# Kernel tuning notes

Measured on AMD Instinct MI355X. Metric: run time of the kernel, lower is better.

The kernel has to match this reference:

```python
import jax, jax.numpy as jnp
import numpy as np

MAX_IT = 20
LAMBDA_ROF = 7.0
SIGMA = 1.0 / (7.0 * 0.01)
TAU = 0.01
THETA = 0.5

H, W_DIM = 4096, 4096


def forward_weighted_gradient(x, w):
    # x: (1,H,W), w: (2,H,W) -> (2,H,W)
    x0 = x[0]
    gh = jnp.pad(x0[:, 1:] - x0[:, :-1], ((0, 0), (0, 1)))   # grad[0,:, :-1]
    gv = jnp.pad(x0[1:, :] - x0[:-1, :], ((0, 1), (0, 0)))   # grad[1,:-1,:]
    return jnp.stack([gh, gv], axis=0) * w


def backward_divergence(y):
    # y: (2,H,W) -> (1,H,W)
    yh, yv = y[0], y[1]
    d_h = jnp.concatenate(
        [yh[:, :1], yh[:, 1:-1] - yh[:, :-2], -yh[:, -2:-1]], axis=1)
    d_v = jnp.concatenate(
        [yv[:1, :], yv[1:-1, :] - yv[:-2, :], -yv[-2:-1, :]], axis=0)
    return (d_h + d_v)[None]


def prox_linf_ball(p, r):
    # p - detach(max(p-r,0) - max(-p-r,0))  (clamp treated as data in torch code)
    shrink = jnp.maximum(p - r, 0.0) - jnp.maximum(-p - r, 0.0)
    return p - jax.lax.stop_gradient(shrink)


def setup_inputs() -> dict:
    key = jax.random.key(0)
    k1, _ = jax.random.split(key)
    img_obs = jax.random.uniform(k1, (1, H, W_DIM), dtype=jnp.float32)
    w = jnp.ones((2, H, W_DIM), dtype=jnp.float32)
    return {"img_obs": img_obs, "w": w}


def reference(img_obs, w):
    x0 = img_obs
    x_tilde0 = img_obs
    y0 = jnp.zeros((2,) + img_obs.shape[1:], dtype=img_obs.dtype)

    def step(carry, _):
        x, x_tilde, y = carry
        y = y + SIGMA * forward_weighted_gradient(x_tilde, w)
        y = prox_linf_ball(y, 1.0)
        x_old = x
        x = (x + TAU * backward_divergence(y)
             + LAMBDA_ROF * TAU * img_obs) / (1.0 + LAMBDA_ROF * TAU)
        x_tilde = x + THETA * (x - x_old)
        return (x, x_tilde, y), None

    (x, x_tilde, y), _ = jax.lax.scan(step, (x0, x_tilde0, y0), None, length=MAX_IT)
    return x_tilde
```

## Files before the change

### kernel.cpp

```cpp
#include <hip/hip_runtime.h>

static constexpr int H = 4096;
static constexpr int W = 4096;
static constexpr long N = (long)H * W;

static constexpr int TILE = 64;
static constexpr int HOFF = 12;
static constexpr int R    = TILE + 2*HOFF;
static constexpr int CPR  = R / 8;
static constexpr int PR   = R / 2;
static constexpr int NTASK= PR * CPR;
static constexpr int PSE  = PR * R;
static constexpr int NT   = 512;

static constexpr float SIGMA = 14.285714285714286f;
static constexpr float INVD  = 1.0f / 1.07f;
static constexpr float TIV   = 0.01f / 1.07f;
static constexpr float CF    = 0.07f / 1.07f;

typedef _Float16 half8  __attribute__((ext_vector_type(8)));
typedef _Float16 half4v __attribute__((ext_vector_type(4)));

__device__ __forceinline__ half8 splat8(float f) {
    _Float16 h = (_Float16)f;
    half8 v = {h, h, h, h, h, h, h, h};
    return v;
}
__device__ __forceinline__ half8 clamp8(half8 v) {
    v = __builtin_elementwise_min(v, splat8(1.0f));
    v = __builtin_elementwise_max(v, splat8(-1.0f));
    return v;
}
__device__ __forceinline__ half4v lo4(half8 v) {
    half4v r = {v[0], v[1], v[2], v[3]}; return r;
}
__device__ __forceinline__ half4v hi4(half8 v) {
    half4v r = {v[4], v[5], v[6], v[7]}; return r;
}

__global__ __launch_bounds__(256) void pack_w(
    const float* __restrict__ wg,
    _Float16* __restrict__ whp, _Float16* __restrict__ wvp)
{
    const long p = ((long)blockIdx.x * 256 + threadIdx.x) * 8;
    const int i = (int)(p >> 12);
    const float4* hp = reinterpret_cast<const float4*>(wg + p);
    float4 a = hp[0], b = hp[1];
    const float4* vp = reinterpret_cast<const float4*>(wg + N + p);
    float4 c = vp[0], d = vp[1];
    float wh[8] = {a.x, a.y, a.z, a.w, b.x, b.y, b.z, b.w};
    float wv[8] = {c.x, c.y, c.z, c.w, d.x, d.y, d.z, d.w};
    half8 whv, wvv;
#pragma unroll
    for (int k = 0; k < 8; ++k) {
        whv[k] = (_Float16)(SIGMA * wh[k]);
        wvv[k] = (_Float16)(SIGMA * wv[k]);
    }
    if ((p & 4095) + 8 == W) whv[7] = (_Float16)0.0f;
    if (i == H - 1) wvv = splat8(0.0f);
    *reinterpret_cast<half8*>(whp + p) = whv;
    *reinterpret_cast<half8*>(wvp + p) = wvv;
}

template<int PHASE>
__global__ __launch_bounds__(NT, 4) void fused_pd(
    const float* __restrict__ img,
    const _Float16* __restrict__ whp, const _Float16* __restrict__ wvp,
    _Float16* __restrict__ cig,
    _Float16* __restrict__ xg, _Float16* __restrict__ yhg, _Float16* __restrict__ yvg,
    float* __restrict__ out)
{
    __shared__ _Float16 lds_s[2 * PSE + 3 * (NTASK + 2)];
    _Float16* __restrict__ xte  = lds_s;
    _Float16* __restrict__ yvo  = lds_s + PSE;
    _Float16* __restrict__ yheA = lds_s + 2 * PSE;
    _Float16* __restrict__ yheB = yheA + (NTASK + 2);
    _Float16* __restrict__ xteo = yheB + (NTASK + 2);

    const int tid = threadIdx.x;
    const bool act = tid < NTASK;
    const int t  = act ? tid : 0;
    const int p  = t / CPR;
    const int j0 = (t - p * CPR) * 8;
    const int be = p * R + j0;
    const int gi0 = blockIdx.y * TILE - HOFF;
    const int gj0 = blockIdx.x * TILE - HOFF;
    const bool interior = (gi0 >= 0) && (gj0 >= 0) && (gi0 + R <= H) && (gj0 + R <= W);

    const half8 kTIV  = splat8(TIV);
    const half8 kINVD = splat8(INVD);
    const half8 k15   = splat8(1.5f);
    const half8 kM05  = splat8(-0.5f);

    half8 wh0, wh1, wv0, wv1;
    half8 ci0, ci1;
    half8 x0, x1;
    half8 xt0r, xt1r;
    half8 yh0, yh1, yv0, yv1;

    auto loadRow = [&](int gi, int gj, half8& whr, half8& wvr, half8& cir,
                       half8& xr, half8& yhr, half8& yvr) {
        if (interior) {
            const long o = (long)gi * W + gj;
            whr = *reinterpret_cast<const half8*>(whp + o);
            wvr = *reinterpret_cast<const half8*>(wvp + o);
            if (PHASE == 0) {
                const float4* ip = reinterpret_cast<const float4*>(img + o);
                float4 a = ip[0], b = ip[1];
                float im[8] = {a.x, a.y, a.z, a.w, b.x, b.y, b.z, b.w};
#pragma unroll
                for (int k = 0; k < 8; ++k) {
                    cir[k] = (_Float16)(CF * im[k]);
                    xr[k]  = (_Float16)im[k];
                }
                yhr = splat8(0.f); yvr = splat8(0.f);
            } else {
                cir = *reinterpret_cast<const half8*>(cig + o);
                xr  = *reinterpret_cast<const half8*>(xg  + o);
                yhr = *reinterpret_cast<const half8*>(yhg + o);
                yvr = *reinterpret_cast<const half8*>(yvg + o);
            }
        } else {
            const int gic = min(max(gi, 0), H - 1);
            const bool rowin = (gi >= 0) && (gi < H);
#pragma unroll
            for (int k = 0; k < 8; ++k) {
                const int gjk = gj + k;
                const int gjc = min(max(gjk, 0), W - 1);
                const bool inim = rowin && (gjk >= 0) && (gjk < W);
                const long o = (long)gic * W + gjc;
                whr[k] = inim ? whp[o] : (_Float16)0.0f;
                wvr[k] = inim ? wvp[o] : (_Float16)0.0f;
                if (PHASE == 0) {
                    const float imf = img[o];
                    cir[k] = (_Float16)(CF * imf);
                    xr[k]  = (_Float16)imf;
                    yhr[k] = (_Float16)0.0f;
                    yvr[k] = (_Float16)0.0f;
                } else {
                    cir[k] = cig[o];
                    xr[k]  = xg[o];
                    yhr[k] = inim ? yhg[o] : (_Float16)0.0f;
                    yvr[k] = inim ? yvg[o] : (_Float16)0.0f;
                }
            }
        }
    };
    if (act) {
        const int gi = gi0 + 2 * p;
        const int gj = gj0 + j0;
        loadRow(gi,     gj, wh0, wv0, ci0, x0, yh0, yv0);
        loadRow(gi + 1, gj, wh1, wv1, ci1, x1, yh1, yv1);
        if (PHASE == 0) {
            xt0r = x0; xt1r = x1;
            *reinterpret_cast<half8*>(xte + be) = xt0r;
            *reinterpret_cast<half8*>(yvo + be) = splat8(0.f);
            xteo[t] = xt1r[0];
            yheA[1 + t] = (_Float16)0.0f;
            yheB[1 + t] = (_Float16)0.0f;
        } else {
            *reinterpret_cast<half8*>(yvo + be) = yv1;
            yheA[1 + t] = yh0[7];
            yheB[1 + t] = yh1[7];
        }
    }
    if (tid == NT - 1) {
        yheA[0] = (_Float16)0.0f;
        yheB[0] = (_Float16)0.0f;
        xteo[NTASK]     = (_Float16)0.0f;
        xteo[NTASK + 1] = (_Float16)0.0f;
    }
    __syncthreads();

    auto dual_all = [&](bool writes) {
        if (act) {
            _Float16 rt0 = xte[be + 8];
            _Float16 rt1 = xteo[t + 1];
            half8 bv1 = *reinterpret_cast<const half8*>(xte + be + R);
            half8 sh0 = __builtin_shufflevector(xt0r, xt0r, 1, 2, 3, 4, 5, 6, 7, 7);
            sh0[7] = rt0;
            half8 sh1 = __builtin_shufflevector(xt1r, xt1r, 1, 2, 3, 4, 5, 6, 7, 7);
            sh1[7] = rt1;
            yh0 = clamp8((sh0 - xt0r) * wh0 + yh0);
            yv0 = clamp8((xt1r - xt0r) * wv0 + yv0);
            yh1 = clamp8((sh1 - xt1r) * wh1 + yh1);
            yv1 = clamp8((bv1 - xt1r) * wv1 + yv1);
            if (writes) {
                *reinterpret_cast<half8*>(yvo + be) = yv1;
                yheA[1 + t] = yh0[7];
                yheB[1 + t] = yh1[7];
            }
        }
    };
    auto prim_all = [&](bool writes) {
        if (act) {
            _Float16 yl0 = yheA[t];
            _Float16 yl1 = yheB[t];
            half8 yva0 = *reinterpret_cast<const half8*>(yvo + be - R);
            half8 ysh0 = __builtin_shufflevector(yh0, yh0, 0, 0, 1, 2, 3, 4, 5, 6);
            ysh0[0] = yl0;
            half8 ysh1 = __builtin_shufflevector(yh1, yh1, 0, 0, 1, 2, 3, 4, 5, 6);
            ysh1[0] = yl1;
            half8 dv0 = (yh0 - ysh0) + (yv0 - yva0);
            half8 dv1 = (yh1 - ysh1) + (yv1 - yv0);
            half8 tt0 = dv0 * kTIV + ci0;
            half8 xn0 = x0 * kINVD + tt0;
            half8 xtn0 = xn0 * k15 + x0 * kM05;
            x0 = xn0; xt0r = xtn0;
            half8 tt1 = dv1 * kTIV + ci1;
            half8 xn1 = x1 * kINVD + tt1;
            half8 xtn1 = xn1 * k15 + x1 * kM05;
            x1 = xn1; xt1r = xtn1;
            if (writes) {
                *reinterpret_cast<half8*>(xte + be) = xt0r;
                xteo[t] = xt1r[0];
            }
        }
    };

    if (PHASE == 1) {
        prim_all(true);
        __syncthreads();
    }
    const int NIT = (PHASE == 0) ? 10 : 9;
    for (int it = 0; it < NIT; ++it) {
        dual_all(true);
        __syncthreads();
        prim_all(!(PHASE == 1 && it == NIT - 1));
        __syncthreads();
    }
    if (PHASE == 0) {
        dual_all(false);
    }

    if (act && p >= 6 && p < 38 && j0 >= 8 && j0 <= 72) {
        const long g0 = (long)(gi0 + 2 * p) * W + (gj0 + j0);
        const long g1 = g0 + W;
        if (PHASE == 0) {
            if (j0 >= 16 && j0 <= 64) {
                *reinterpret_cast<half8*>(xg  + g0) = x0;
                *reinterpret_cast<half8*>(xg  + g1) = x1;
                *reinterpret_cast<half8*>(yhg + g0) = yh0;
                *reinterpret_cast<half8*>(yhg + g1) = yh1;
                *reinterpret_cast<half8*>(yvg + g0) = yv0;
                *reinterpret_cast<half8*>(yvg + g1) = yv1;
                *reinterpret_cast<half8*>(cig + g0) = ci0;
                *reinterpret_cast<half8*>(cig + g1) = ci1;
            } else if (j0 == 8) {
                *reinterpret_cast<half4v*>(xg  + g0 + 4) = hi4(x0);
                *reinterpret_cast<half4v*>(xg  + g1 + 4) = hi4(x1);
                *reinterpret_cast<half4v*>(yhg + g0 + 4) = hi4(yh0);
                *reinterpret_cast<half4v*>(yhg + g1 + 4) = hi4(yh1);
                *reinterpret_cast<half4v*>(yvg + g0 + 4) = hi4(yv0);
                *reinterpret_cast<half4v*>(yvg + g1 + 4) = hi4(yv1);
                *reinterpret_cast<half4v*>(cig + g0 + 4) = hi4(ci0);
                *reinterpret_cast<half4v*>(cig + g1 + 4) = hi4(ci1);
            } else {
                *reinterpret_cast<half4v*>(xg  + g0) = lo4(x0);
                *reinterpret_cast<half4v*>(xg  + g1) = lo4(x1);
                *reinterpret_cast<half4v*>(yhg + g0) = lo4(yh0);
                *reinterpret_cast<half4v*>(yhg + g1) = lo4(yh1);
                *reinterpret_cast<half4v*>(yvg + g0) = lo4(yv0);
                *reinterpret_cast<half4v*>(yvg + g1) = lo4(yv1);
                *reinterpret_cast<half4v*>(cig + g0) = lo4(ci0);
                *reinterpret_cast<half4v*>(cig + g1) = lo4(ci1);
            }
        } else {
            float4 a0 = make_float4((float)xt0r[0], (float)xt0r[1], (float)xt0r[2], (float)xt0r[3]);
            float4 a1 = make_float4((float)xt0r[4], (float)xt0r[5], (float)xt0r[6], (float)xt0r[7]);
            float4 b0 = make_float4((float)xt1r[0], (float)xt1r[1], (float)xt1r[2], (float)xt1r[3]);
            float4 b1 = make_float4((float)xt1r[4], (float)xt1r[5], (float)xt1r[6], (float)xt1r[7]);
            if (j0 >= 16 && j0 <= 64) {
                *reinterpret_cast<float4*>(out + g0)     = a0;
                *reinterpret_cast<float4*>(out + g0 + 4) = a1;
                *reinterpret_cast<float4*>(out + g1)     = b0;
                *reinterpret_cast<float4*>(out + g1 + 4) = b1;
            } else if (j0 == 8) {
                *reinterpret_cast<float4*>(out + g0 + 4) = a1;
                *reinterpret_cast<float4*>(out + g1 + 4) = b1;
            } else {
                *reinterpret_cast<float4*>(out + g0) = a0;
                *reinterpret_cast<float4*>(out + g1) = b0;
            }
        }
    }
}

extern "C" void kernel_launch(void* const* d_in, const int* in_sizes, int n_in,
                              void* d_out, int out_size, void* d_ws, size_t ws_size,
                              hipStream_t stream) {
    const float* img = (const float*)d_in[0];
    const float* wg  = (const float*)d_in[1];
    float* out = (float*)d_out;

    _Float16* ws16 = (_Float16*)d_ws;
    _Float16* whp = ws16;
    _Float16* wvp = ws16 + N;
    _Float16* cig = ws16 + 2 * N;
    _Float16* xg  = ws16 + 3 * N;
    _Float16* yhg = ws16 + 4 * N;
    _Float16* yvg = ws16 + 5 * N;

    pack_w<<<dim3((int)(N / 8 / 256)), dim3(256), 0, stream>>>(wg, whp, wvp);

    dim3 grid(W / TILE, H / TILE);
    fused_pd<0><<<grid, dim3(NT), 0, stream>>>(img, whp, wvp, cig, xg, yhg, yvg, out);
    fused_pd<1><<<grid, dim3(NT), 0, stream>>>(img, whp, wvp, cig, xg, yhg, yvg, out);
}
```

Before: 337.2 us.

## Recompute neighbor dual values redundantly and double-buffer x_tilde to halve barriers

Each thread now loads its upper and left neighbor weights and dual values and recomputes those neighbor dual updates itself, so it no longer exchanges dual values through LDS. Only x_tilde is shared, through ping-pong LDS buffers, which drops one of the two __syncthreads per iteration. The cost is extra redundant dual arithmetic, extra global loads for the halo terms, and more registers per thread, which could lower occupancy.

```diff
diff --git a/kernel.cpp b/kernel.cpp
--- a/kernel.cpp
+++ b/kernel.cpp
@@ -12,6 +12,8 @@
 static constexpr int NTASK= PR * CPR;
 static constexpr int PSE  = PR * R;
 static constexpr int NT   = 512;
+static constexpr int PAD  = 8;
+static constexpr int BUFH = 2 * PSE + 2 * PAD;
 
 static constexpr float SIGMA = 14.285714285714286f;
 static constexpr float INVD  = 1.0f / 1.07f;
@@ -20,6 +22,7 @@
 
 typedef _Float16 half8  __attribute__((ext_vector_type(8)));
 typedef _Float16 half4v __attribute__((ext_vector_type(4)));
+typedef _Float16 half2v __attribute__((ext_vector_type(2)));
 
 __device__ __forceinline__ half8 splat8(float f) {
     _Float16 h = (_Float16)f;
@@ -29,6 +32,13 @@
 __device__ __forceinline__ half8 clamp8(half8 v) {
     v = __builtin_elementwise_min(v, splat8(1.0f));
     v = __builtin_elementwise_max(v, splat8(-1.0f));
+    return v;
+}
+__device__ __forceinline__ half2v clamp2(half2v v) {
+    half2v one  = {(_Float16)1.0f, (_Float16)1.0f};
+    half2v mone = {(_Float16)-1.0f, (_Float16)-1.0f};
+    v = __builtin_elementwise_min(v, one);
+    v = __builtin_elementwise_max(v, mone);
     return v;
 }
 __device__ __forceinline__ half4v lo4(half8 v) {
@@ -70,12 +80,11 @@
     _Float16* __restrict__ xg, _Float16* __restrict__ yhg, _Float16* __restrict__ yvg,
     float* __restrict__ out)
 {
-    __shared__ _Float16 lds_s[2 * PSE + 3 * (NTASK + 2)];
-    _Float16* __restrict__ xte  = lds_s;
-    _Float16* __restrict__ yvo  = lds_s + PSE;
-    _Float16* __restrict__ yheA = lds_s + 2 * PSE;
-    _Float16* __restrict__ yheB = yheA + (NTASK + 2);
-    _Float16* __restrict__ xteo = yheB + (NTASK + 2);
+    __shared__ _Float16 lds_s[2 * BUFH];
+    _Float16* const xteA = lds_s + PAD;
+    _Float16* const xtoA = xteA + PSE;
+    _Float16* const xteB = lds_s + BUFH + PAD;
+    _Float16* const xtoB = xteB + PSE;
 
     const int tid = threadIdx.x;
     const bool act = tid < NTASK;
@@ -97,6 +106,8 @@
     half8 x0, x1;
     half8 xt0r, xt1r;
     half8 yh0, yh1, yv0, yv1;
+    half8 wva, yva;
+    half2v whl, yhl;
 
     auto loadRow = [&](int gi, int gj, half8& whr, half8& wvr, half8& cir,
                        half8& xr, half8& yhr, half8& yvr) {
@@ -151,57 +162,74 @@
         const int gj = gj0 + j0;
         loadRow(gi,     gj, wh0, wv0, ci0, x0, yh0, yv0);
         loadRow(gi + 1, gj, wh1, wv1, ci1, x1, yh1, yv1);
-        if (PHASE == 0) {
-            xt0r = x0; xt1r = x1;
-            *reinterpret_cast<half8*>(xte + be) = xt0r;
-            *reinterpret_cast<half8*>(yvo + be) = splat8(0.f);
-            xteo[t] = xt1r[0];
-            yheA[1 + t] = (_Float16)0.0f;
-            yheB[1 + t] = (_Float16)0.0f;
+        if (interior) {
+            const long om = (long)(gi - 1) * W + gj;
+            wva = *reinterpret_cast<const half8*>(wvp + om);
+            whl[0] = whp[(long)gi * W + gj - 1];
+            whl[1] = whp[(long)(gi + 1) * W + gj - 1];
+            if (PHASE == 1) {
+                yva = *reinterpret_cast<const half8*>(yvg + om);
+                yhl[0] = yhg[(long)gi * W + gj - 1];
+                yhl[1] = yhg[(long)(gi + 1) * W + gj - 1];
+            } else {
+                yva = splat8(0.f);
+                yhl[0] = (_Float16)0.0f; yhl[1] = (_Float16)0.0f;
+            }
         } else {
-            *reinterpret_cast<half8*>(yvo + be) = yv1;
-            yheA[1 + t] = yh0[7];
-            yheB[1 + t] = yh1[7];
-        }
-    }
-    if (tid == NT - 1) {
-        yheA[0] = (_Float16)0.0f;
-        yheB[0] = (_Float16)0.0f;
-        xteo[NTASK]     = (_Float16)0.0f;
-        xteo[NTASK + 1] = (_Float16)0.0f;
-    }
-    __syncthreads();
-
-    auto dual_all = [&](bool writes) {
+            const int gim = gi - 1;
+            const bool rowm = (gim >= 0) && (gim < H);
+#pragma unroll
+            for (int k = 0; k < 8; ++k) {
+                const int gjk = gj + k;
+                const bool inm = rowm && (gjk >= 0) && (gjk < W);
+                const long o = (long)min(max(gim, 0), H - 1) * W + min(max(gjk, 0), W - 1);
+                wva[k] = inm ? wvp[o] : (_Float16)0.0f;
+                yva[k] = (PHASE == 1 && inm) ? yvg[o] : (_Float16)0.0f;
+            }
+            const int gjl = gj - 1;
+            const bool incol = (gjl >= 0) && (gjl < W);
+            const bool inl0 = incol && (gi >= 0) && (gi < H);
+            const bool inl1 = incol && (gi + 1 >= 0) && (gi + 1 < H);
+            const long ol0 = (long)min(max(gi, 0), H - 1) * W + min(max(gjl, 0), W - 1);
+            const long ol1 = (long)min(max(gi + 1, 0), H - 1) * W + min(max(gjl, 0), W - 1);
+            whl[0] = inl0 ? whp[ol0] : (_Float16)0.0f;
+            whl[1] = inl1 ? whp[ol1] : (_Float16)0.0f;
+            yhl[0] = (PHASE == 1 && inl0) ? yhg[ol0] : (_Float16)0.0f;
+            yhl[1] = (PHASE == 1 && inl1) ? yhg[ol1] : (_Float16)0.0f;
+        }
+    }
+
+    auto dual_all = [&](const _Float16* xe, const _Float16* xo, bool red) {
         if (act) {
-            _Float16 rt0 = xte[be + 8];
-            _Float16 rt1 = xteo[t + 1];
-            half8 bv1 = *reinterpret_cast<const half8*>(xte + be + R);
+            _Float16 rt0 = xe[be + 8];
+            _Float16 rt1 = xo[be + 8];
+            half8 bv1 = *reinterpret_cast<const half8*>(xe + be + R);
             half8 sh0 = __builtin_shufflevector(xt0r, xt0r, 1, 2, 3, 4, 5, 6, 7, 7);
             sh0[7] = rt0;
             half8 sh1 = __builtin_shufflevector(xt1r, xt1r, 1, 2, 3, 4, 5, 6, 7, 7);
             sh1[7] = rt1;
+            if (red) {
+                half8 xta = *reinterpret_cast<const half8*>(xo + be - R);
+                _Float16 xtl0 = xe[be - 1];
+                _Float16 xtl1 = xo[be - 1];
+                yva = clamp8((xt0r - xta) * wva + yva);
+                half2v xf; xf[0] = xt0r[0]; xf[1] = xt1r[0];
+                half2v xl; xl[0] = xtl0;   xl[1] = xtl1;
+                yhl = clamp2((xf - xl) * whl + yhl);
+            }
             yh0 = clamp8((sh0 - xt0r) * wh0 + yh0);
             yv0 = clamp8((xt1r - xt0r) * wv0 + yv0);
             yh1 = clamp8((sh1 - xt1r) * wh1 + yh1);
             yv1 = clamp8((bv1 - xt1r) * wv1 + yv1);
-            if (writes) {
-                *reinterpret_cast<half8*>(yvo + be) = yv1;
-                yheA[1 + t] = yh0[7];
-                yheB[1 + t] = yh1[7];
-            }
         }
     };
-    auto prim_all = [&](bool writes) {
+    auto prim_all = [&]() {
         if (act) {
-            _Float16 yl0 = yheA[t];
-            _Float16 yl1 = yheB[t];
-            half8 yva0 = *reinterpret_cast<const half8*>(yvo + be - R);
             half8 ysh0 = __builtin_shufflevector(yh0, yh0, 0, 0, 1, 2, 3, 4, 5, 6);
-            ysh0[0] = yl0;
+            ysh0[0] = yhl[0];
             half8 ysh1 = __builtin_shufflevector(yh1, yh1, 0, 0, 1, 2, 3, 4, 5, 6);
-            ysh1[0] = yl1;
-            half8 dv0 = (yh0 - ysh0) + (yv0 - yva0);
+            ysh1[0] = yhl[1];
+            half8 dv0 = (yh0 - ysh0) + (yv0 - yva);
             half8 dv1 = (yh1 - ysh1) + (yv1 - yv0);
             half8 tt0 = dv0 * kTIV + ci0;
             half8 xn0 = x0 * kINVD + tt0;
@@ -211,26 +239,44 @@
             half8 xn1 = x1 * kINVD + tt1;
             half8 xtn1 = xn1 * k15 + x1 * kM05;
             x1 = xn1; xt1r = xtn1;
-            if (writes) {
-                *reinterpret_cast<half8*>(xte + be) = xt0r;
-                xteo[t] = xt1r[0];
-            }
         }
     };
 
-    if (PHASE == 1) {
-        prim_all(true);
-        __syncthreads();
-    }
+    if (PHASE == 0) {
+        if (act) {
+            xt0r = x0; xt1r = x1;
+            *reinterpret_cast<half8*>(xteA + be) = xt0r;
+            *reinterpret_cast<half8*>(xtoA + be) = xt1r;
+        }
+    } else {
+        prim_all();
+        if (act) {
+            *reinterpret_cast<half8*>(xteA + be) = xt0r;
+            *reinterpret_cast<half8*>(xtoA + be) = xt1r;
+        }
+    }
+    __syncthreads();
+
     const int NIT = (PHASE == 0) ? 10 : 9;
     for (int it = 0; it < NIT; ++it) {
-        dual_all(true);
-        __syncthreads();
-        prim_all(!(PHASE == 1 && it == NIT - 1));
-        __syncthreads();
+        const bool even = (it & 1) == 0;
+        const _Float16* xeR = even ? xteA : xteB;
+        const _Float16* xoR = even ? xtoA : xtoB;
+        _Float16* xeW = even ? xteB : xteA;
+        _Float16* xoW = even ? xtoB : xtoA;
+        dual_all(xeR, xoR, true);
+        prim_all();
+        if (!(PHASE == 1 && it == NIT - 1)) {
+            if (act) {
+                *reinterpret_cast<half8*>(xeW + be) = xt0r;
+                *reinterpret_cast<half8*>(xoW + be) = xt1r;
+            }
+            __syncthreads();
+        }
     }
     if (PHASE == 0) {
-        dual_all(false);
+        const _Float16* xeR = ((NIT & 1) == 0) ? xteA : xteB;
+        dual_all(xeR, xeR + PSE, false);
     }
 
     if (act && p >= 6 && p < 38 && j0 >= 8 && j0 <= 72) {
```

After: 412.8 us. 22.4% more time.
